# Performance work log

Measured on AMD Instinct MI355X. Metric: run time of the kernel, lower is better.

Reference implementation:

```python
import jax, jax.numpy as jnp
import numpy as np
from jax import lax

# dims: T timesteps, CIN=6 DoG channels, HxW image; F conv filters, K kernel
T, CIN, H, W_IN = 15, 6, 512, 512
F, K, PAD = 64, 5, 2
THRESH = 15.0
K_WTA, RADIUS = 5, 2  # self.k1, self.r1


def setup_inputs() -> dict:
    key = jax.random.key(0)
    k1, k2 = jax.random.split(key)
    # cumulative binary spike wave: once a unit spikes it stays 1 (SpykeTorch convention)
    ev = (jax.random.uniform(k1, (T, CIN, H, W_IN)) < 0.02).astype(jnp.float32)
    x = jnp.clip(jnp.cumsum(ev, axis=0), 0.0, 1.0)
    w = 0.8 + 0.05 * jax.random.normal(k2, (F, CIN, K, K), dtype=jnp.float32)
    return {"x": x, "w": w}


def _pool_pad(x, pad):
    # sf.pooling(x, 2, 2): max-pool 2x2 stride 2; sf.pad: zero pad
    x = lax.reduce_window(x, -jnp.inf, lax.max, (1, 1, 2, 2), (1, 1, 2, 2), 'VALID')
    return jnp.pad(x, ((0, 0), (0, 0), (pad, pad), (pad, pad)))


def _fire(pot, thr):
    # sf.fire(pot, thr, True): zero sub-threshold potentials, spikes = sign
    tp = jnp.where(pot < thr, 0.0, pot)
    return jnp.sign(tp), tp


def _pointwise_inhibition(pot):
    # keep, per spatial site, only the feature with the earliest (then strongest) spike
    T_ = pot.shape[0]
    max_vals = jnp.max(pot, axis=1, keepdims=True)      # [T,1,H,W]
    max_idx = jnp.argmax(pot, axis=1, keepdims=True)    # [T,1,H,W]
    clamp = jnp.sign(max_vals)                          # 1 where any feature active
    earliest = jnp.clip(T_ - jnp.sum(clamp, axis=0, keepdims=True), 0, T_ - 1).astype(jnp.int32)  # [1,1,H,W]
    winners = jnp.take_along_axis(max_idx, earliest, axis=0)  # [1,1,H,W] winning feature
    has_spike = clamp[-1:]                              # [1,1,H,W] any spike by last step
    ch = jnp.arange(pot.shape[1]).reshape(1, -1, 1, 1)
    coef = jnp.where(ch == winners, has_spike, 0.0)     # scatter of winner coeff
    return pot * coef


def _get_k_winners(pot, spikes, k, radius):
    # NMS-like radius-based k-winners-take-all over [F,H,W]
    T_ = pot.shape[0]
    earliest = jnp.clip(T_ - jnp.sum(spikes, axis=0, keepdims=True), 0, T_ - 1).astype(jnp.int32)
    values = jnp.take_along_axis(pot, earliest, axis=0)  # potential at earliest spike
    trunc = spikes * values
    v = jnp.max(trunc) * T_  # large bias favoring earlier spikes
    total = jnp.sum(trunc + spikes * v, axis=0)          # [F,H,W]
    Fc, Hh, Ww = total.shape
    feat = jnp.arange(Fc).reshape(-1, 1, 1)
    row = jnp.arange(Hh).reshape(1, -1, 1)
    col = jnp.arange(Ww).reshape(1, 1, -1)
    winners = []
    for _ in range(k):  # small fixed k (5), fine to unroll
        idx = jnp.argmax(total)
        val = jnp.reshape(total, (-1,))[idx]
        f, r, c = jnp.unravel_index(idx, total.shape)
        active = val != 0
        win = jnp.where(active, jnp.stack([f, r, c]).astype(jnp.int32),
                        jnp.full((3,), -1, jnp.int32))
        winners.append(win)
        suppress = (feat == f) | ((jnp.abs(row - r) <= radius) & (jnp.abs(col - c) <= radius))
        total = jnp.where(active & suppress, 0.0, total)
    return jnp.stack(winners)  # [k,3] with -1 rows when fewer winners exist


def reference(x, w):
    inp = _pool_pad(x, PAD)  # [T,6,260,260]
    pot = lax.conv_general_dilated(inp, w, (1, 1), 'VALID',
                                   dimension_numbers=('NCHW', 'OIHW', 'NCHW'))  # [T,F,256,256]
    spk, pot = _fire(pot, THRESH)
    pot = _pointwise_inhibition(pot)
    spk = jnp.sign(pot)
    winners = _get_k_winners(pot, spk, K_WTA, RADIUS)
    return spk, winners
```

## Files before the change

### kernel.cpp

```cpp
#include <hip/hip_runtime.h>
#include <hip/hip_bf16.h>

#define T_ 15
#define CIN_ 6
#define F_ 64
#define HW_ 256
#define PW_ 260
#define THRESH_ 15.0f
#define TAU_NEVER 15


__global__ __launch_bounds__(256) void pool_tau(const float* __restrict__ x,
                                                unsigned char* __restrict__ tau,
                                                unsigned long long* __restrict__ slots,
                                                unsigned int* __restrict__ gmaxp) {
    int idx = blockIdx.x * 256 + threadIdx.x;
    if (idx < 5) slots[idx] = 0ULL;
    if (idx == 5) *gmaxp = 0u;
    if (idx >= CIN_ * PW_ * PW_) return;
    int xx = idx % PW_;
    int rest = idx / PW_;
    int yy = rest % PW_;
    int c = rest / PW_;
    unsigned char tv = TAU_NEVER;
    if (xx >= 2 && xx < 258 && yy >= 2 && yy < 258) {
        int i = yy - 2, j = xx - 2;
        const float* b0 = x + ((size_t)c * 512 + 2 * i) * 512 + 2 * j;
        const size_t tstride = (size_t)CIN_ * 512 * 512;
        {
            const float* b = b0 + 14 * tstride;
            float2 a = *(const float2*)b;
            float2 d = *(const float2*)(b + 512);
            if (a.x > 0.f || a.y > 0.f || d.x > 0.f || d.y > 0.f) {
                int lo = 0, hi = 14;
                while (lo < hi) {
                    int mid = (lo + hi) >> 1;
                    const float* bm = b0 + (size_t)mid * tstride;
                    float2 am = *(const float2*)bm;
                    float2 dm = *(const float2*)(bm + 512);
                    bool on = (am.x > 0.f || am.y > 0.f || dm.x > 0.f || dm.y > 0.f);
                    if (on) hi = mid; else lo = mid + 1;
                }
                tv = (unsigned char)lo;
            }
        }
    }
    tau[idx] = tv;
}

__global__ __launch_bounds__(256, 3) void phaseA(const unsigned char* __restrict__ tau,
                                                 const float* __restrict__ w,
                                                 int* __restrict__ rec_wch,
                                                 float* __restrict__ rec_val,
                                                 int* __restrict__ rec_e,
                                                 unsigned int* __restrict__ gmaxp) {
    __shared__ float wl2[150 * 64];
    __shared__ unsigned char tw[CIN_ * 144];
    __shared__ float wmax[4];

    const int tid = threadIdx.x;
    const int lane = tid & 63;
    const int g = tid >> 6;
    const int gx = (g & 1) * 4;
    const int gy = (g >> 1) * 4;
    const int px0 = blockIdx.x * 8;
    const int py0 = blockIdx.y * 8;

    for (int idx = tid; idx < 9600; idx += 256) {
        int k = idx >> 6, f = idx & 63;
        wl2[idx] = w[f * 150 + k];
    }
    for (int idx = tid; idx < CIN_ * 144; idx += 256) {
        int c = idx / 144;
        int rem = idx - c * 144;
        int r = rem / 12;
        int xx = rem - r * 12;
        tw[idx] = tau[(c * PW_ + (py0 + r)) * PW_ + (px0 + xx)];
    }
    __syncthreads();

    unsigned int done = 0;
    int myw = -1, mye = T_;
    float myv = 0.0f;
    float wavemax = 0.0f;

    for (int t = 0; t < T_; ++t) {
        float acc[16];
#pragma unroll
        for (int i = 0; i < 16; ++i) acc[i] = 0.0f;

        for (int c = 0; c < CIN_; ++c) {
            float win[8][8];
            const unsigned char* tb = &tw[c * 144 + gy * 12 + gx];
#pragma unroll
            for (int r = 0; r < 8; ++r) {
                unsigned int lo = *(const unsigned int*)(tb + r * 12);
                unsigned int hi = *(const unsigned int*)(tb + r * 12 + 4);
#pragma unroll
                for (int b = 0; b < 4; ++b) {
                    win[r][b]     = (((lo >> (8 * b)) & 0xFF) <= (unsigned)t) ? 1.0f : 0.0f;
                    win[r][4 + b] = (((hi >> (8 * b)) & 0xFF) <= (unsigned)t) ? 1.0f : 0.0f;
                }
            }
#pragma unroll
            for (int ki = 0; ki < 5; ++ki)
#pragma unroll
                for (int kj = 0; kj < 5; ++kj) {
                    float wv = wl2[((c * 25 + ki * 5 + kj) << 6) + lane];
#pragma unroll
                    for (int py = 0; py < 4; ++py)
#pragma unroll
                        for (int px = 0; px < 4; ++px)
                            acc[py * 4 + px] += win[py + ki][px + kj] * wv;
                }
        }

#pragma unroll
        for (int i = 0; i < 16; ++i) {
            if (done & (1u << i)) continue;
            float v = acc[i];
            v = (v < THRESH_) ? 0.0f : v;
            if (__any(v > 0.0f)) {
                unsigned long long key =
                    ((unsigned long long)__float_as_uint(v) << 6) | (unsigned)(63 - lane);
#pragma unroll
                for (int m = 1; m < 64; m <<= 1) {
                    unsigned long long o = __shfl_xor(key, m, 64);
                    if (o > key) key = o;
                }
                float mv = __uint_as_float((unsigned int)(key >> 6));
                int wf = 63 - (int)(key & 63ULL);
                done |= (1u << i);
                if (lane == i) { myw = wf; myv = mv; mye = t; }
                wavemax = fmaxf(wavemax, mv);
            }
        }
        if (done == 0xFFFFu) break;
    }

    if (lane < 16) {
        int py = lane >> 2, px = lane & 3;
        int p = (py0 + gy + py) * HW_ + (px0 + gx + px);
        rec_wch[p] = myw;
        rec_val[p] = myv;
        rec_e[p] = mye;
    }
    if (lane == 0) wmax[g] = wavemax;
    __syncthreads();
    if (tid == 0) {
        float m = fmaxf(fmaxf(wmax[0], wmax[1]), fmaxf(wmax[2], wmax[3]));
        if (m > 0.0f) atomicMax(gmaxp, __float_as_uint(m));
    }
}

__global__ __launch_bounds__(256) void render(const int* __restrict__ rec_wch,
                                              const int* __restrict__ rec_e,
                                              float* __restrict__ out) {
    const int tid = threadIdx.x;
    const int t = blockIdx.y;
    const int px = blockIdx.x * 1024 + tid * 4;

    int4 wch4 = *(const int4*)(rec_wch + px);
    int4 e4   = *(const int4*)(rec_e + px);
    int s0 = (wch4.x >= 0 && t >= e4.x) ? wch4.x : -1;
    int s1 = (wch4.y >= 0 && t >= e4.y) ? wch4.y : -1;
    int s2 = (wch4.z >= 0 && t >= e4.z) ? wch4.z : -1;
    int s3 = (wch4.w >= 0 && t >= e4.w) ? wch4.w : -1;

    float* base = out + (((size_t)t * F_) << 16) + px;
#pragma unroll
    for (int f = 0; f < F_; ++f) {
        float4 v;
        v.x = (f == s0) ? 1.0f : 0.0f;
        v.y = (f == s1) ? 1.0f : 0.0f;
        v.z = (f == s2) ? 1.0f : 0.0f;
        v.w = (f == s3) ? 1.0f : 0.0f;
        *(float4*)(base + ((size_t)f << 16)) = v;
    }
}

__global__ __launch_bounds__(256) void compute_total(const int* __restrict__ rec_wch,
                                                     const float* __restrict__ rec_val,
                                                     const int* __restrict__ rec_e,
                                                     const unsigned int* __restrict__ gmaxp,
                                                     float* __restrict__ total) {
    int i = blockIdx.x * 256 + threadIdx.x;
    int wch = rec_wch[i];
    float g = __uint_as_float(*gmaxp);
    float v15 = 15.0f * g;
    float tot = 0.0f;
    if (wch >= 0) {
        int e = rec_e[i];
        float base = rec_val[i] + v15;
        for (int t = e; t < T_; ++t) tot += base;
    }
    total[i] = tot;
}

__global__ __launch_bounds__(256) void max_round(const float* __restrict__ total,
                                                 const int* __restrict__ rec_wch,
                                                 unsigned long long* __restrict__ slots,
                                                 int round) {
    __shared__ unsigned long long sred[256];
    int i = blockIdx.x * 256 + threadIdx.x;
    float v = total[i];
    unsigned long long key = 0ULL;
    if (v > 0.0f) {
        int fch = rec_wch[i];
        int r = i >> 8, c = i & 255;
        bool sup = false;
        for (int j = 0; j < round; ++j) {
            unsigned long long s = slots[j];
            if (s == 0ULL) continue;
            int fl = 0x7fffffff - (int)(unsigned int)(s & 0xffffffffu);
            int fj = fl >> 16, rj = (fl >> 8) & 255, cj = fl & 255;
            int dr = r - rj; if (dr < 0) dr = -dr;
            int dc = c - cj; if (dc < 0) dc = -dc;
            if (fch == fj || (dr <= 2 && dc <= 2)) sup = true;
        }
        if (!sup) {
            int fl = (fch << 16) | i;
            unsigned int comp = 0x7fffffffu - (unsigned int)fl;
            key = ((unsigned long long)__float_as_uint(v) << 32) | comp;
        }
    }
    sred[threadIdx.x] = key;
    __syncthreads();
    for (int s = 128; s > 0; s >>= 1) {
        if (threadIdx.x < s) {
            if (sred[threadIdx.x + s] > sred[threadIdx.x]) sred[threadIdx.x] = sred[threadIdx.x + s];
        }
        __syncthreads();
    }
    if (threadIdx.x == 0 && sred[0] != 0ULL)
        atomicMax(&slots[round], sred[0]);
}

__global__ void writer(const unsigned long long* __restrict__ slots,
                       float* __restrict__ out) {
    int r = threadIdx.x;
    if (r < 5) {
        unsigned long long s = slots[r];
        float* wout = out + (size_t)T_ * F_ * HW_ * HW_ + r * 3;
        if (s != 0ULL) {
            int fl = 0x7fffffff - (int)(unsigned int)(s & 0xffffffffu);
            wout[0] = (float)(fl >> 16);
            wout[1] = (float)((fl >> 8) & 255);
            wout[2] = (float)(fl & 255);
        } else {
            wout[0] = -1.0f; wout[1] = -1.0f; wout[2] = -1.0f;
        }
    }
}

extern "C" void kernel_launch(void* const* d_in, const int* in_sizes, int n_in,
                              void* d_out, int out_size, void* d_ws, size_t ws_size,
                              hipStream_t stream) {
    const float* x = (const float*)d_in[0];
    const float* w = (const float*)d_in[1];
    float* out = (float*)d_out;

    char* wsc = (char*)d_ws;
    unsigned char* tau = (unsigned char*)wsc;
    size_t off = (size_t)CIN_ * PW_ * PW_;
    int* rec_wch = (int*)(wsc + off);        off += 65536 * sizeof(int);
    float* rec_val = (float*)(wsc + off);    off += 65536 * sizeof(float);
    int* rec_e = (int*)(wsc + off);          off += 65536 * sizeof(int);
    float* total = (float*)(wsc + off);      off += 65536 * sizeof(float);
    unsigned long long* slots = (unsigned long long*)(wsc + off);  off += 5 * sizeof(unsigned long long);
    unsigned int* gmaxp = (unsigned int*)(wsc + off);

    pool_tau<<<(CIN_ * PW_ * PW_ + 255) / 256, 256, 0, stream>>>(x, tau, slots, gmaxp);
    phaseA<<<dim3(32, 32), 256, 0, stream>>>(tau, w, rec_wch, rec_val, rec_e, gmaxp);
    render<<<dim3(64, 15), 256, 0, stream>>>(rec_wch, rec_e, out);
    compute_total<<<256, 256, 0, stream>>>(rec_wch, rec_val, rec_e, gmaxp, total);
    for (int r = 0; r < 5; ++r)
        max_round<<<256, 256, 0, stream>>>(total, rec_wch, slots, r);
    writer<<<1, 64, 0, stream>>>(slots, out);
}
```

Measured before the change: 471.4 us.

## Fuse k-WTA total, rounds and writer into one single-block kernel

Replaces the compute_total kernel, five max_round launches and the writer kernel with one 1024-thread block. The block keeps all 65536 keys in registers, runs the five argmax-and-suppress rounds with wave shuffles and LDS, and writes the winners itself. This removes six kernel launches, the global total buffer, the slots buffer and the atomics. In exchange it runs on a single CU with 64 64-bit keys per thread, which is heavy register pressure and may spill.

```diff
diff --git a/kernel.cpp b/kernel.cpp
--- a/kernel.cpp
+++ b/kernel.cpp
@@ -1,5 +1,4 @@
 #include <hip/hip_runtime.h>
-#include <hip/hip_bf16.h>
 
 #define T_ 15
 #define CIN_ 6
@@ -12,11 +11,9 @@
 
 __global__ __launch_bounds__(256) void pool_tau(const float* __restrict__ x,
                                                 unsigned char* __restrict__ tau,
-                                                unsigned long long* __restrict__ slots,
                                                 unsigned int* __restrict__ gmaxp) {
     int idx = blockIdx.x * 256 + threadIdx.x;
-    if (idx < 5) slots[idx] = 0ULL;
-    if (idx == 5) *gmaxp = 0u;
+    if (idx == 0) *gmaxp = 0u;
     if (idx >= CIN_ * PW_ * PW_) return;
     int xx = idx % PW_;
     int rest = idx / PW_;
@@ -179,76 +176,95 @@
     }
 }
 
-__global__ __launch_bounds__(256) void compute_total(const int* __restrict__ rec_wch,
-                                                     const float* __restrict__ rec_val,
-                                                     const int* __restrict__ rec_e,
-                                                     const unsigned int* __restrict__ gmaxp,
-                                                     float* __restrict__ total) {
-    int i = blockIdx.x * 256 + threadIdx.x;
-    int wch = rec_wch[i];
-    float g = __uint_as_float(*gmaxp);
-    float v15 = 15.0f * g;
-    float tot = 0.0f;
-    if (wch >= 0) {
-        int e = rec_e[i];
-        float base = rec_val[i] + v15;
-        for (int t = e; t < T_; ++t) tot += base;
-    }
-    total[i] = tot;
-}
-
-__global__ __launch_bounds__(256) void max_round(const float* __restrict__ total,
-                                                 const int* __restrict__ rec_wch,
-                                                 unsigned long long* __restrict__ slots,
-                                                 int round) {
-    __shared__ unsigned long long sred[256];
-    int i = blockIdx.x * 256 + threadIdx.x;
-    float v = total[i];
-    unsigned long long key = 0ULL;
-    if (v > 0.0f) {
+__global__ __launch_bounds__(1024) void kwta(const int* __restrict__ rec_wch,
+                                             const float* __restrict__ rec_val,
+                                             const int* __restrict__ rec_e,
+                                             const unsigned int* __restrict__ gmaxp,
+                                             float* __restrict__ out) {
+    __shared__ unsigned long long lred[16];
+    __shared__ unsigned long long lwin;
+    const int tid = threadIdx.x;
+    const int lane = tid & 63;
+    const int wv = tid >> 6;
+    const float v15 = 15.0f * __uint_as_float(*gmaxp);
+
+    unsigned long long keys[64];
+    unsigned long long alive = 0ULL;
+#pragma unroll
+    for (int k = 0; k < 64; ++k) {
+        int i = k * 1024 + tid;
         int fch = rec_wch[i];
-        int r = i >> 8, c = i & 255;
-        bool sup = false;
-        for (int j = 0; j < round; ++j) {
-            unsigned long long s = slots[j];
-            if (s == 0ULL) continue;
+        unsigned long long key = 0ULL;
+        if (fch >= 0) {
+            int e = rec_e[i];
+            float base = rec_val[i] + v15;
+            float tot = 0.0f;
+            for (int t = e; t < T_; ++t) tot += base;
+            if (tot > 0.0f) {
+                unsigned int comp = 0x7fffffffu - (unsigned int)((fch << 16) | i);
+                key = ((unsigned long long)__float_as_uint(tot) << 32) | comp;
+            }
+        }
+        keys[k] = key;
+        if (key != 0ULL) alive |= (1ULL << k);
+    }
+
+    const int mycol = tid & 255;
+    const int rowbase = tid >> 8;
+    int wf[5], wr[5], wc[5];
+
+#pragma unroll
+    for (int round = 0; round < 5; ++round) {
+        unsigned long long mymax = 0ULL;
+#pragma unroll
+        for (int k = 0; k < 64; ++k) {
+            unsigned long long kk = ((alive >> k) & 1ULL) ? keys[k] : 0ULL;
+            if (kk > mymax) mymax = kk;
+        }
+#pragma unroll
+        for (int m = 1; m < 64; m <<= 1) {
+            unsigned long long o = __shfl_xor(mymax, m, 64);
+            if (o > mymax) mymax = o;
+        }
+        if (lane == 0) lred[wv] = mymax;
+        __syncthreads();
+        if (wv == 0) {
+            unsigned long long v = (lane < 16) ? lred[lane] : 0ULL;
+#pragma unroll
+            for (int m = 1; m < 16; m <<= 1) {
+                unsigned long long o = __shfl_xor(v, m, 64);
+                if (o > v) v = o;
+            }
+            if (lane == 0) lwin = v;
+        }
+        __syncthreads();
+        unsigned long long s = lwin;
+        if (s != 0ULL) {
             int fl = 0x7fffffff - (int)(unsigned int)(s & 0xffffffffu);
             int fj = fl >> 16, rj = (fl >> 8) & 255, cj = fl & 255;
-            int dr = r - rj; if (dr < 0) dr = -dr;
-            int dc = c - cj; if (dc < 0) dc = -dc;
-            if (fch == fj || (dr <= 2 && dc <= 2)) sup = true;
-        }
-        if (!sup) {
-            int fl = (fch << 16) | i;
-            unsigned int comp = 0x7fffffffu - (unsigned int)fl;
-            key = ((unsigned long long)__float_as_uint(v) << 32) | comp;
-        }
-    }
-    sred[threadIdx.x] = key;
-    __syncthreads();
-    for (int s = 128; s > 0; s >>= 1) {
-        if (threadIdx.x < s) {
-            if (sred[threadIdx.x + s] > sred[threadIdx.x]) sred[threadIdx.x] = sred[threadIdx.x + s];
-        }
-        __syncthreads();
-    }
-    if (threadIdx.x == 0 && sred[0] != 0ULL)
-        atomicMax(&slots[round], sred[0]);
-}
-
-__global__ void writer(const unsigned long long* __restrict__ slots,
-                       float* __restrict__ out) {
-    int r = threadIdx.x;
-    if (r < 5) {
-        unsigned long long s = slots[r];
-        float* wout = out + (size_t)T_ * F_ * HW_ * HW_ + r * 3;
-        if (s != 0ULL) {
-            int fl = 0x7fffffff - (int)(unsigned int)(s & 0xffffffffu);
-            wout[0] = (float)(fl >> 16);
-            wout[1] = (float)((fl >> 8) & 255);
-            wout[2] = (float)(fl & 255);
+            wf[round] = fj; wr[round] = rj; wc[round] = cj;
+            int dc = mycol - cj; if (dc < 0) dc = -dc;
+            const bool colhit = (dc <= 2);
+#pragma unroll
+            for (int k = 0; k < 64; ++k) {
+                if (!((alive >> k) & 1ULL)) continue;
+                int flk = 0x7fffffff - (int)(unsigned int)(keys[k] & 0xffffffffu);
+                int fck = flk >> 16;
+                int dr = (k * 4 + rowbase) - rj; if (dr < 0) dr = -dr;
+                if (fck == fj || (colhit && dr <= 2)) alive &= ~(1ULL << k);
+            }
         } else {
-            wout[0] = -1.0f; wout[1] = -1.0f; wout[2] = -1.0f;
+            wf[round] = -1; wr[round] = -1; wc[round] = -1;
+        }
+    }
+
+    if (tid == 0) {
+        float* wout = out + (size_t)T_ * F_ * HW_ * HW_;
+#pragma unroll
+        for (int r = 0; r < 5; ++r) {
+            wout[r * 3 + 0] = (float)wf[r];
+            wout[r * 3 + 1] = (float)wr[r];
+            wout[r * 3 + 2] = (float)wc[r];
         }
     }
 }
@@ -266,15 +282,10 @@
     int* rec_wch = (int*)(wsc + off);        off += 65536 * sizeof(int);
     float* rec_val = (float*)(wsc + off);    off += 65536 * sizeof(float);
     int* rec_e = (int*)(wsc + off);          off += 65536 * sizeof(int);
-    float* total = (float*)(wsc + off);      off += 65536 * sizeof(float);
-    unsigned long long* slots = (unsigned long long*)(wsc + off);  off += 5 * sizeof(unsigned long long);
     unsigned int* gmaxp = (unsigned int*)(wsc + off);
 
-    pool_tau<<<(CIN_ * PW_ * PW_ + 255) / 256, 256, 0, stream>>>(x, tau, slots, gmaxp);
+    pool_tau<<<(CIN_ * PW_ * PW_ + 255) / 256, 256, 0, stream>>>(x, tau, gmaxp);
     phaseA<<<dim3(32, 32), 256, 0, stream>>>(tau, w, rec_wch, rec_val, rec_e, gmaxp);
     render<<<dim3(64, 15), 256, 0, stream>>>(rec_wch, rec_e, out);
-    compute_total<<<256, 256, 0, stream>>>(rec_wch, rec_val, rec_e, gmaxp, total);
-    for (int r = 0; r < 5; ++r)
-        max_round<<<256, 256, 0, stream>>>(total, rec_wch, slots, r);
-    writer<<<1, 64, 0, stream>>>(slots, out);
-}
+    kwta<<<1, 1024, 0, stream>>>(rec_wch, rec_val, rec_e, gmaxp, out);
+}
```

New measurement: 688.0 us. +45.9%, slower.
